# Optimization experiments

Hardware: AMD Instinct MI355X
Metric: run time of the kernel (lower is better)

## Reference

```python
import jax, jax.numpy as jnp
import numpy as np

BIG = 3.4028234e+38  # torch fill value used as additive mask
EPS = 1e-5           # nn.LayerNorm default eps


def _layernorm(x):
    mu = jnp.mean(x, axis=-1, keepdims=True)
    var = jnp.mean(jnp.square(x - mu), axis=-1, keepdims=True)
    return (x - mu) / jnp.sqrt(var + EPS)


def setup_inputs() -> dict:
    key = jax.random.key(0)
    ks = jax.random.split(key, 12)
    B, N, H, S = 32, 512, 256, 3  # batch, num_codes, embedding_size, num_stacks
    features = jax.random.normal(ks[0], (B, N, H), dtype=jnp.float32)
    masks = jnp.ones((B, N, 1), dtype=jnp.float32)
    guide = jax.random.randint(ks[1], (B, N, N), 0, 2).astype(jnp.float32)
    prior_guide = jax.random.uniform(ks[2], (B, N, N), dtype=jnp.float32)
    sc = 0.02
    WQ = jax.random.normal(ks[3], (S, H, H), dtype=jnp.float32) * sc
    WK = jax.random.normal(ks[4], (S, H, H), dtype=jnp.float32) * sc
    WV = jax.random.normal(ks[5], (S, H, H), dtype=jnp.float32) * sc
    W1 = jax.random.normal(ks[6], (S, H, H), dtype=jnp.float32) * sc
    b1 = jnp.zeros((S, H), dtype=jnp.float32)
    W2 = jax.random.normal(ks[7], (S, H, H), dtype=jnp.float32) * sc
    b2 = jnp.zeros((S, H), dtype=jnp.float32)
    return {"features": features, "masks": masks, "guide": guide,
            "prior_guide": prior_guide, "WQ": WQ, "WK": WK, "WV": WV,
            "W1": W1, "b1": b1, "W2": W2, "b2": b2}


def reference(features, masks, guide, prior_guide, WQ, WK, WV, W1, b1, W2, b2):
    H = features.shape[-1]
    scale = 1.0 / jnp.sqrt(jnp.float32(H))
    attention_mask = jnp.where(masks[:, :, 0] != 0, 0.0, BIG)  # [B,N]
    inf_mask = jnp.where(guide != 0, 0.0, BIG)                 # [B,N,N]
    attentions = []
    x = features
    for i in range(WQ.shape[0]):
        f = masks * x                                          # [B,N,H]
        if i == 0:
            att = prior_guide[:, None, :, :]                   # use_prior path
        else:
            q = jnp.einsum('bnh,hd->bnd', f, WQ[i].T)          # nn.Linear: x @ W^T
            k = jnp.einsum('bnh,hd->bnd', f, WK[i].T)
            pre = jnp.einsum('bqd,bkd->bqk', q, k) * scale     # [B,N,N] (heads=1)
            pre = pre - attention_mask[:, None, :] - inf_mask
            att = jax.nn.softmax(pre, axis=-1)[:, None, :, :]  # [B,1,N,N]
        attentions.append(att)
        v = jnp.einsum('bnh,hd->bnd', f, WV[i].T)              # [B,N,H]
        post = jnp.einsum('bqk,bkh->bqh', att[:, 0], v)        # squeeze head dim
        post = _layernorm(post + f)
        ffn = jnp.maximum(jnp.einsum('bnh,hd->bnd', post, W1[i].T) + b1[i], 0.0)
        ffn = jnp.einsum('bnh,hd->bnd', ffn, W2[i].T) + b2[i]
        x = _layernorm(ffn + post)
    return x * masks, jnp.stack(attentions)
```

## Files before the change

kernel.cpp:

```cpp
#include <hip/hip_runtime.h>
#include <cstdint>
#include <cstddef>

#define B_ 32
#define N_ 512
#define H_ 256
#define S_ 3
#define BN_ (B_*N_)
#define HH_ (H_*H_)
#define BIGF 3.4028234e+38f
#define EPSF 1e-5f

typedef __bf16 bf16x8 __attribute__((ext_vector_type(8)));
typedef float  f32x4  __attribute__((ext_vector_type(4)));

typedef const void __attribute__((address_space(1)))* gas_t;
typedef void __attribute__((address_space(3)))* las_t;

__device__ __forceinline__ void async16(const unsigned short* g, unsigned short* l) {
  __builtin_amdgcn_global_load_lds((gas_t)g, (las_t)l, 16, 0, 0);
}

__device__ __forceinline__ unsigned short f2bf(float f) {
  __bf16 h = (__bf16)f;
  unsigned short s;
  __builtin_memcpy(&s, &h, 2);
  return s;
}
__device__ __forceinline__ float bf2f(unsigned short u) {
  unsigned int v = ((unsigned int)u) << 16;
  float f;
  __builtin_memcpy(&f, &v, 4);
  return f;
}

#define KC_STAGE(lane) ((((lane) & 3) ^ (((lane) >> 3) & 3)) * 8)
#define KC_READ(quad, l15) ((((quad) ^ (((l15) >> 1) & 3))) * 8)

__global__ __launch_bounds__(256) void cvt_all_k(
    const float* __restrict__ WQ, const float* __restrict__ WK,
    const float* __restrict__ WV, const float* __restrict__ W1,
    const float* __restrict__ W2,
    unsigned short* __restrict__ wqk, unsigned short* __restrict__ wv,
    unsigned short* __restrict__ w1, unsigned short* __restrict__ w2) {
  const int per = S_ * HH_ / 4;
  int gi = blockIdx.x * 256 + threadIdx.x;
  int which = gi / per;
  int e4 = gi - which * per;
  float4 v;
  if      (which == 0) v = ((const float4*)WQ)[e4];
  else if (which == 1) v = ((const float4*)WK)[e4];
  else if (which == 2) v = ((const float4*)WV)[e4];
  else if (which == 3) v = ((const float4*)W1)[e4];
  else                 v = ((const float4*)W2)[e4];
  ushort4 o;
  o.x = f2bf(v.x); o.y = f2bf(v.y); o.z = f2bf(v.z); o.w = f2bf(v.w);
  int e = e4 * 4;
  if (which <= 1) {
    int L = e / HH_, off = e - L * HH_;
    *(ushort4*)&wqk[(size_t)L * 2 * HH_ + (which == 1 ? HH_ : 0) + off] = o;
  } else if (which == 2) ((ushort4*)wv)[e4] = o;
  else if   (which == 3) ((ushort4*)w1)[e4] = o;
  else                   ((ushort4*)w2)[e4] = o;
}

__global__ __launch_bounds__(256) void mask_mul_k(
    const float* __restrict__ x, const float* __restrict__ masks,
    unsigned short* __restrict__ fb) {
  int i = blockIdx.x * 256 + threadIdx.x;
  int row = i >> 6;
  float m = masks[row];
  float4 v = ((const float4*)x)[i];
  ushort4 o;
  o.x = f2bf(v.x * m); o.y = f2bf(v.y * m); o.z = f2bf(v.z * m); o.w = f2bf(v.w * m);
  ((ushort4*)fb)[i] = o;
}

__global__ __launch_bounds__(256) void mfma_gemm_k(
    const unsigned short* __restrict__ A, const unsigned short* __restrict__ Bm,
    unsigned short* __restrict__ Cb,
    int K, int Nn, int lda, int ldb, long sA, long sB, long sC) {
  __shared__ __align__(16) unsigned short As[2][128 * 32];
  __shared__ __align__(16) unsigned short Bs[2][128 * 32];
  const int b = blockIdx.z;
  const int t = threadIdx.x;
  const int wave = t >> 6, lane = t & 63;
  const int wm = wave >> 1, wn = wave & 1;
  const int quad = lane >> 4, l15 = lane & 15;
  const int m0 = blockIdx.y * 128, n0 = blockIdx.x * 128;
  const int srow = lane >> 2;
  const int kc = KC_STAGE(lane);
  const int pos8 = (lane & 3) * 8;

  const unsigned short* pa0 = A + (size_t)b * sA + (size_t)(m0 + wave * 32 + srow) * lda + kc;
  const unsigned short* pa1 = pa0 + 16 * (size_t)lda;
  const unsigned short* pb0 = Bm + (size_t)b * sB + (size_t)(n0 + wave * 32 + srow) * ldb + kc;
  const unsigned short* pb1 = pb0 + 16 * (size_t)ldb;
  const int lo = (wave * 32 + srow) * 32 + pos8;

  f32x4 acc[4][4];
#pragma unroll
  for (int i = 0; i < 4; ++i)
#pragma unroll
    for (int j = 0; j < 4; ++j) acc[i][j] = (f32x4){0.f, 0.f, 0.f, 0.f};

  const int soff = KC_READ(quad, l15);
  const int NT = K >> 5;
  async16(pa0, &As[0][lo]); async16(pa1, &As[0][lo + 16 * 32]);
  async16(pb0, &Bs[0][lo]); async16(pb1, &Bs[0][lo + 16 * 32]);
  __syncthreads();
  int cur = 0;
  for (int tt = 0; tt < NT; ++tt) {
    if (tt + 1 < NT) {
      const int kn = (tt + 1) << 5;
      async16(pa0 + kn, &As[cur ^ 1][lo]); async16(pa1 + kn, &As[cur ^ 1][lo + 16 * 32]);
      async16(pb0 + kn, &Bs[cur ^ 1][lo]); async16(pb1 + kn, &Bs[cur ^ 1][lo + 16 * 32]);
    }
    bf16x8 af[4], bfr[4];
#pragma unroll
    for (int i = 0; i < 4; ++i)
      af[i] = *(const bf16x8*)&As[cur][(wm * 64 + i * 16 + l15) * 32 + soff];
#pragma unroll
    for (int j = 0; j < 4; ++j)
      bfr[j] = *(const bf16x8*)&Bs[cur][(wn * 64 + j * 16 + l15) * 32 + soff];
#pragma unroll
    for (int i = 0; i < 4; ++i)
#pragma unroll
      for (int j = 0; j < 4; ++j)
        acc[i][j] = __builtin_amdgcn_mfma_f32_16x16x32_bf16(af[i], bfr[j], acc[i][j], 0, 0, 0);
    __syncthreads();
    cur ^= 1;
  }

#pragma unroll
  for (int i = 0; i < 4; ++i) {
    const int rbase = m0 + wm * 64 + i * 16 + quad * 4;
#pragma unroll
    for (int j = 0; j < 4; ++j) {
      const int c = n0 + wn * 64 + j * 16 + l15;
#pragma unroll
      for (int r = 0; r < 4; ++r)
        Cb[(size_t)b * sC + (size_t)(rbase + r) * Nn + c] = f2bf(acc[i][j][r]);
    }
  }
}

template<int PRIOR>
__global__ __launch_bounds__(512) void ls_pv_k(
    const unsigned short* __restrict__ qk, const float* __restrict__ prior,
    const float* __restrict__ masks, const float* __restrict__ guide,
    const unsigned short* __restrict__ vT, const unsigned short* __restrict__ resb,
    float* __restrict__ att, float* __restrict__ post, unsigned short* __restrict__ postb) {
  __shared__ __align__(16) unsigned short As[2][64 * 32];
  __shared__ __align__(16) unsigned short Bs[2][512 * 32];
  __shared__ __align__(16) unsigned short Ps[64 * 520];
  __shared__ float red[4][64][2];
  const int b = blockIdx.x;
  const int t = threadIdx.x;
  const int wave = t >> 6, lane = t & 63;
  const int quad = lane >> 4, l15 = lane & 15;
  const int m0 = blockIdx.y * 64;
  const int srow = lane >> 2;
  const int kc = KC_STAGE(lane);
  const int pos8 = (lane & 3) * 8;
  const int soff = KC_READ(quad, l15);

  const unsigned short* vb = vT + (size_t)b * H_ * N_;
  const unsigned short* pv0 = vb + (size_t)(wave * 16 + srow) * N_ + kc;
  const unsigned short* pv1 = pv0 + (size_t)128 * N_;
  const int lvo = (wave * 16 + srow) * 32 + pos8;

  if (PRIOR) {
    async16(pv0, &Bs[0][lvo]);
    async16(pv1, &Bs[0][lvo + 128 * 32]);
    const float* src = prior + ((size_t)b * N_ + m0) * N_;
    float*       dst = att   + ((size_t)b * N_ + m0) * N_;
#pragma unroll
    for (int s = 0; s < 16; ++s) {
      int idx4 = s * 512 + t;
      float4 v = ((const float4*)src)[idx4];
      ((float4*)dst)[idx4] = v;
      int row = idx4 >> 7, col4 = idx4 & 127;
      ushort4 o;
      o.x = f2bf(v.x); o.y = f2bf(v.y); o.z = f2bf(v.z); o.w = f2bf(v.w);
      *(ushort4*)&Ps[row * 520 + col4 * 4] = o;
    }
    __syncthreads();
  } else {
    const int wm = wave >> 2, wn = wave & 3;
    const int ld = 2 * H_;
    const unsigned short* base = qk + (size_t)b * N_ * ld;
    const unsigned short* pa = base + (size_t)(m0 + wave * 16 + srow) * ld + kc;
    const unsigned short* pb = base + H_ + (size_t)(wave * 64 + srow) * ld + kc;
    const int lao = (wave * 16 + srow) * 32 + pos8;
    const int lbo = (wave * 64 + srow) * 32 + pos8;

    f32x4 acc[2][8];
#pragma unroll
    for (int i = 0; i < 2; ++i)
#pragma unroll
      for (int j = 0; j < 8; ++j) acc[i][j] = (f32x4){0.f, 0.f, 0.f, 0.f};

    if (wave < 4) async16(pa, &As[0][lao]);
#pragma unroll
    for (int c = 0; c < 4; ++c)
      async16(pb + (size_t)c * 16 * ld, &Bs[0][lbo + c * 16 * 32]);
    __syncthreads();
    int cur = 0;
#pragma unroll
    for (int tt = 0; tt < 8; ++tt) {
      if (tt < 7) {
        const int kn = (tt + 1) * 32;
        if (wave < 4) async16(pa + kn, &As[cur ^ 1][lao]);
#pragma unroll
        for (int c = 0; c < 4; ++c)
          async16(pb + (size_t)c * 16 * ld + kn, &Bs[cur ^ 1][lbo + c * 16 * 32]);
      }
      bf16x8 af[2], bfr[8];
#pragma unroll
      for (int i = 0; i < 2; ++i)
        af[i] = *(const bf16x8*)&As[cur][(wm * 32 + i * 16 + l15) * 32 + soff];
#pragma unroll
      for (int j = 0; j < 8; ++j)
        bfr[j] = *(const bf16x8*)&Bs[cur][(wn * 128 + j * 16 + l15) * 32 + soff];
#pragma unroll
      for (int i = 0; i < 2; ++i)
#pragma unroll
        for (int j = 0; j < 8; ++j)
          acc[i][j] = __builtin_amdgcn_mfma_f32_16x16x32_bf16(af[i], bfr[j], acc[i][j], 0, 0, 0);
      __syncthreads();
      cur ^= 1;
    }

    async16(pv0, &Bs[0][lvo]);
    async16(pv1, &Bs[0][lvo + 128 * 32]);

    float am[8];
#pragma unroll
    for (int j = 0; j < 8; ++j) {
      float mv = masks[(size_t)b * N_ + wn * 128 + j * 16 + l15];
      am[j] = (mv != 0.f) ? 0.f : BIGF;
    }
#pragma unroll
    for (int i = 0; i < 2; ++i) {
#pragma unroll
      for (int r = 0; r < 4; ++r) {
        const int mloc = wm * 32 + i * 16 + quad * 4 + r;
        const float* gr = guide + ((size_t)b * N_ + m0 + mloc) * N_;
        float mx = -BIGF;
#pragma unroll
        for (int j = 0; j < 8; ++j) {
          const int c = wn * 128 + j * 16 + l15;
          float g = gr[c];
          float v = acc[i][j][r] * 0.0625f - am[j] - ((g != 0.f) ? 0.f : BIGF);
          acc[i][j][r] = v;
          mx = fmaxf(mx, v);
        }
#pragma unroll
        for (int off = 1; off < 16; off <<= 1) mx = fmaxf(mx, __shfl_xor(mx, off));
        if (l15 == 0) red[wn][mloc][0] = mx;
      }
    }
    __syncthreads();
#pragma unroll
    for (int i = 0; i < 2; ++i) {
#pragma unroll
      for (int r = 0; r < 4; ++r) {
        const int mloc = wm * 32 + i * 16 + quad * 4 + r;
        float M = fmaxf(fmaxf(red[0][mloc][0], red[1][mloc][0]),
                        fmaxf(red[2][mloc][0], red[3][mloc][0]));
        float s = 0.f;
#pragma unroll
        for (int j = 0; j < 8; ++j) {
          float e = __expf(acc[i][j][r] - M);
          acc[i][j][r] = e;
          s += e;
        }
#pragma unroll
        for (int off = 1; off < 16; off <<= 1) s += __shfl_xor(s, off);
        if (l15 == 0) red[wn][mloc][1] = s;
      }
    }
    __syncthreads();
#pragma unroll
    for (int i = 0; i < 2; ++i) {
#pragma unroll
      for (int r = 0; r < 4; ++r) {
        const int mloc = wm * 32 + i * 16 + quad * 4 + r;
        float S = red[0][mloc][1] + red[1][mloc][1] + red[2][mloc][1] + red[3][mloc][1];
        float inv = 1.f / S;
        const size_t rowoff = ((size_t)b * N_ + m0 + mloc) * N_;
#pragma unroll
        for (int j = 0; j < 8; ++j) {
          const int c = wn * 128 + j * 16 + l15;
          float o = acc[i][j][r] * inv;
          att[rowoff + c] = o;
          Ps[mloc * 520 + c] = f2bf(o);
        }
      }
    }
    __syncthreads();
  }

  const int wm2 = wave >> 2, wn2 = wave & 3;

  f32x4 acc2[2][4];
#pragma unroll
  for (int i = 0; i < 2; ++i)
#pragma unroll
    for (int j = 0; j < 4; ++j) acc2[i][j] = (f32x4){0.f, 0.f, 0.f, 0.f};

  int cur = 0;
#pragma unroll
  for (int tt = 0; tt < 16; ++tt) {
    if (tt < 15) {
      const int kn = (tt + 1) * 32;
      async16(pv0 + kn, &Bs[cur ^ 1][lvo]);
      async16(pv1 + kn, &Bs[cur ^ 1][lvo + 128 * 32]);
    }
    bf16x8 af[2], bfr[4];
#pragma unroll
    for (int i = 0; i < 2; ++i)
      af[i] = *(const bf16x8*)&Ps[(wm2 * 32 + i * 16 + l15) * 520 + tt * 32 + quad * 8];
#pragma unroll
    for (int j = 0; j < 4; ++j)
      bfr[j] = *(const bf16x8*)&Bs[cur][(wn2 * 64 + j * 16 + l15) * 32 + soff];
#pragma unroll
    for (int i = 0; i < 2; ++i)
#pragma unroll
      for (int j = 0; j < 4; ++j)
        acc2[i][j] = __builtin_amdgcn_mfma_f32_16x16x32_bf16(af[i], bfr[j], acc2[i][j], 0, 0, 0);
    __syncthreads();
    cur ^= 1;
  }

#pragma unroll
  for (int i = 0; i < 2; ++i) {
#pragma unroll
    for (int r = 0; r < 4; ++r) {
      const int mloc = wm2 * 32 + i * 16 + quad * 4 + r;
      const long grow = (long)b * N_ + m0 + mloc;
      float s = 0.f, q = 0.f;
#pragma unroll
      for (int j = 0; j < 4; ++j) {
        const int c = wn2 * 64 + j * 16 + l15;
        float v = acc2[i][j][r] + bf2f(resb[grow * H_ + c]);
        acc2[i][j][r] = v;
        s += v; q += v * v;
      }
#pragma unroll
      for (int off = 1; off < 16; off <<= 1) {
        s += __shfl_xor(s, off);
        q += __shfl_xor(q, off);
      }
      if (l15 == 0) { red[wn2][mloc][0] = s; red[wn2][mloc][1] = q; }
    }
  }
  __syncthreads();
#pragma unroll
  for (int i = 0; i < 2; ++i) {
#pragma unroll
    for (int r = 0; r < 4; ++r) {
      const int mloc = wm2 * 32 + i * 16 + quad * 4 + r;
      const long grow = (long)b * N_ + m0 + mloc;
      float S = red[0][mloc][0] + red[1][mloc][0] + red[2][mloc][0] + red[3][mloc][0];
      float Q = red[0][mloc][1] + red[1][mloc][1] + red[2][mloc][1] + red[3][mloc][1];
      float mu = S * (1.f / H_);
      float var = Q * (1.f / H_) - mu * mu;
      float inv = 1.f / sqrtf(var + EPSF);
#pragma unroll
      for (int j = 0; j < 4; ++j) {
        const int c = wn2 * 64 + j * 16 + l15;
        float o = (acc2[i][j][r] - mu) * inv;
        post[grow * H_ + c] = o;
        postb[grow * H_ + c] = f2bf(o);
      }
    }
  }
}

template<int LAST>
__global__ __launch_bounds__(512) void ffn_k(
    const unsigned short* __restrict__ postb, const float* __restrict__ postf,
    const unsigned short* __restrict__ w1, const float* __restrict__ b1,
    const unsigned short* __restrict__ w2, const float* __restrict__ b2,
    const float* __restrict__ masks,
    unsigned short* __restrict__ fb, float* __restrict__ outx) {
  __shared__ __align__(16) unsigned short As[2][64 * 32];
  __shared__ __align__(16) unsigned short Bs[2][256 * 32];
  __shared__ __align__(16) unsigned short T1[64 * 264];
  __shared__ float red[4][64][2];
  const int t = threadIdx.x;
  const int wave = t >> 6, lane = t & 63;
  const int wm = wave >> 2, wn = wave & 3;
  const int quad = lane >> 4, l15 = lane & 15;
  const int m0 = blockIdx.y * 64;
  const int srow = lane >> 2;
  const int kc = KC_STAGE(lane);
  const int pos8 = (lane & 3) * 8;
  const int soff = KC_READ(quad, l15);

  const unsigned short* pa = postb + (size_t)(m0 + wave * 16 + srow) * H_ + kc;
  const int lao = (wave * 16 + srow) * 32 + pos8;
  const int lbo = (wave * 16 + srow) * 32 + pos8;

  const unsigned short* qb0 = w2 + (size_t)(wave * 16 + srow) * H_ + kc;
  const unsigned short* qb1 = qb0 + (size_t)128 * H_;

  {
    const unsigned short* pb0 = w1 + (size_t)(wave * 16 + srow) * H_ + kc;
    const unsigned short* pb1 = pb0 + (size_t)128 * H_;
    f32x4 acc[2][4];
#pragma unroll
    for (int i = 0; i < 2; ++i)
#pragma unroll
      for (int j = 0; j < 4; ++j) acc[i][j] = (f32x4){0.f, 0.f, 0.f, 0.f};
    if (wave < 4) async16(pa, &As[0][lao]);
    async16(pb0, &Bs[0][lbo]);
    async16(pb1, &Bs[0][lbo + 128 * 32]);
    __syncthreads();
    int cur = 0;
#pragma unroll
    for (int tt = 0; tt < 8; ++tt) {
      if (tt < 7) {
        const int kn = (tt + 1) * 32;
        if (wave < 4) async16(pa + kn, &As[cur ^ 1][lao]);
        async16(pb0 + kn, &Bs[cur ^ 1][lbo]);
        async16(pb1 + kn, &Bs[cur ^ 1][lbo + 128 * 32]);
      }
      bf16x8 af[2], bfr[4];
#pragma unroll
      for (int i = 0; i < 2; ++i)
        af[i] = *(const bf16x8*)&As[cur][(wm * 32 + i * 16 + l15) * 32 + soff];
#pragma unroll
      for (int j = 0; j < 4; ++j)
        bfr[j] = *(const bf16x8*)&Bs[cur][(wn * 64 + j * 16 + l15) * 32 + soff];
#pragma unroll
      for (int i = 0; i < 2; ++i)
#pragma unroll
        for (int j = 0; j < 4; ++j)
          acc[i][j] = __builtin_amdgcn_mfma_f32_16x16x32_bf16(af[i], bfr[j], acc[i][j], 0, 0, 0);
      __syncthreads();
      cur ^= 1;
    }

    async16(qb0, &Bs[0][lbo]);
    async16(qb1, &Bs[0][lbo + 128 * 32]);

    float bv[4];
#pragma unroll
    for (int j = 0; j < 4; ++j) bv[j] = b1[wn * 64 + j * 16 + l15];
#pragma unroll
    for (int i = 0; i < 2; ++i) {
#pragma unroll
      for (int r = 0; r < 4; ++r) {
        const int mloc = wm * 32 + i * 16 + quad * 4 + r;
#pragma unroll
        for (int j = 0; j < 4; ++j) {
          const int c = wn * 64 + j * 16 + l15;
          T1[mloc * 264 + c] = f2bf(fmaxf(acc[i][j][r] + bv[j], 0.f));
        }
      }
    }
  }
  __syncthreads();

  {
    f32x4 acc[2][4];
#pragma unroll
    for (int i = 0; i < 2; ++i)
#pragma unroll
      for (int j = 0; j < 4; ++j) acc[i][j] = (f32x4){0.f, 0.f, 0.f, 0.f};
    int cur = 0;
#pragma unroll
    for (int tt = 0; tt < 8; ++tt) {
      if (tt < 7) {
        const int kn = (tt + 1) * 32;
        async16(qb0 + kn, &Bs[cur ^ 1][lbo]);
        async16(qb1 + kn, &Bs[cur ^ 1][lbo + 128 * 32]);
      }
      bf16x8 af[2], bfr[4];
#pragma unroll
      for (int i = 0; i < 2; ++i)
        af[i] = *(const bf16x8*)&T1[(wm * 32 + i * 16 + l15) * 264 + tt * 32 + quad * 8];
#pragma unroll
      for (int j = 0; j < 4; ++j)
        bfr[j] = *(const bf16x8*)&Bs[cur][(wn * 64 + j * 16 + l15) * 32 + soff];
#pragma unroll
      for (int i = 0; i < 2; ++i)
#pragma unroll
        for (int j = 0; j < 4; ++j)
          acc[i][j] = __builtin_amdgcn_mfma_f32_16x16x32_bf16(af[i], bfr[j], acc[i][j], 0, 0, 0);
      __syncthreads();
      cur ^= 1;
    }
    float bv[4];
#pragma unroll
    for (int j = 0; j < 4; ++j) bv[j] = b2[wn * 64 + j * 16 + l15];
#pragma unroll
    for (int i = 0; i < 2; ++i) {
#pragma unroll
      for (int r = 0; r < 4; ++r) {
        const int mloc = wm * 32 + i * 16 + quad * 4 + r;
        const long grow = (long)m0 + mloc;
        float s = 0.f, q = 0.f;
#pragma unroll
        for (int j = 0; j < 4; ++j) {
          const int c = wn * 64 + j * 16 + l15;
          float v = acc[i][j][r] + bv[j] + postf[grow * H_ + c];
          acc[i][j][r] = v;
          s += v; q += v * v;
        }
#pragma unroll
        for (int off = 1; off < 16; off <<= 1) {
          s += __shfl_xor(s, off);
          q += __shfl_xor(q, off);
        }
        if (l15 == 0) { red[wn][mloc][0] = s; red[wn][mloc][1] = q; }
      }
    }
    __syncthreads();
#pragma unroll
    for (int i = 0; i < 2; ++i) {
#pragma unroll
      for (int r = 0; r < 4; ++r) {
        const int mloc = wm * 32 + i * 16 + quad * 4 + r;
        const long grow = (long)m0 + mloc;
        float S = red[0][mloc][0] + red[1][mloc][0] + red[2][mloc][0] + red[3][mloc][0];
        float Q = red[0][mloc][1] + red[1][mloc][1] + red[2][mloc][1] + red[3][mloc][1];
        float mu = S * (1.f / H_);
        float var = Q * (1.f / H_) - mu * mu;
        float inv = 1.f / sqrtf(var + EPSF);
        float mval = masks[grow];
#pragma unroll
        for (int j = 0; j < 4; ++j) {
          const int c = wn * 64 + j * 16 + l15;
          float o = (acc[i][j][r] - mu) * inv * mval;
          if (LAST) outx[grow * H_ + c] = o;
          else      fb[grow * H_ + c] = f2bf(o);
        }
      }
    }
  }
}

extern "C" void kernel_launch(void* const* d_in, const int* in_sizes, int n_in,
                              void* d_out, int out_size, void* d_ws, size_t ws_size,
                              hipStream_t stream) {
  const float* features = (const float*)d_in[0];
  const float* masks    = (const float*)d_in[1];
  const float* guide    = (const float*)d_in[2];
  const float* prior    = (const float*)d_in[3];
  const float* WQ       = (const float*)d_in[4];
  const float* WK       = (const float*)d_in[5];
  const float* WV       = (const float*)d_in[6];
  const float* W1       = (const float*)d_in[7];
  const float* b1       = (const float*)d_in[8];
  const float* W2       = (const float*)d_in[9];
  const float* b2       = (const float*)d_in[10];

  float* out     = (float*)d_out;
  float* out_x   = out;
  float* out_att = out + (size_t)BN_ * H_;

  char* w = (char*)d_ws;
  float* post = (float*)w;                     w += (size_t)BN_ * H_ * 4;
  unsigned short* f_bf   = (unsigned short*)w; w += (size_t)BN_ * H_ * 2;
  unsigned short* qk_bf  = (unsigned short*)w; w += (size_t)BN_ * 2 * H_ * 2;
  unsigned short* post_bf= (unsigned short*)w; w += (size_t)BN_ * H_ * 2;
  unsigned short* vT     = (unsigned short*)w; w += (size_t)BN_ * H_ * 2;
  unsigned short* wqk_bf = (unsigned short*)w; w += (size_t)S_ * 2 * HH_ * 2;
  unsigned short* wv_bf  = (unsigned short*)w; w += (size_t)S_ * HH_ * 2;
  unsigned short* w1_bf  = (unsigned short*)w; w += (size_t)S_ * HH_ * 2;
  unsigned short* w2_bf  = (unsigned short*)w; w += (size_t)S_ * HH_ * 2;

  dim3 g_cvt(5 * S_ * HH_ / 1024);
  dim3 g_ew(BN_ * H_ / 1024);
  dim3 g_qkp(4, BN_ / 128, 1);
  dim3 g_vt(4, 2, B_);
  dim3 g_ls(B_, N_ / 64, 1);
  dim3 g_ffn(1, BN_ / 64, 1);

  cvt_all_k<<<g_cvt, 256, 0, stream>>>(WQ, WK, WV, W1, W2, wqk_bf, wv_bf, w1_bf, w2_bf);
  mask_mul_k<<<g_ew, 256, 0, stream>>>(features, masks, f_bf);

  const long sF  = (long)N_ * H_;
  const long sVT = (long)H_ * N_;

  for (int i = 0; i < S_; ++i) {
    float* att = out_att + (size_t)i * B_ * N_ * N_;
    mfma_gemm_k<<<g_vt, 256, 0, stream>>>(wv_bf + (size_t)i * HH_, f_bf, vT,
                                          H_, N_, H_, H_, 0, sF, sVT);
    if (i == 0) {
      ls_pv_k<1><<<g_ls, 512, 0, stream>>>(nullptr, prior, nullptr, nullptr,
                                           vT, f_bf, att, post, post_bf);
    } else {
      mfma_gemm_k<<<g_qkp, 256, 0, stream>>>(f_bf, wqk_bf + (size_t)i * 2 * HH_, qk_bf,
                                             H_, 2 * H_, H_, H_, 0, 0, 0);
      ls_pv_k<0><<<g_ls, 512, 0, stream>>>(qk_bf, nullptr, masks, guide,
                                           vT, f_bf, att, post, post_bf);
    }
    if (i < S_ - 1) {
      ffn_k<0><<<g_ffn, 512, 0, stream>>>(post_bf, post,
          w1_bf + (size_t)i * HH_, b1 + (size_t)i * H_,
          w2_bf + (size_t)i * HH_, b2 + (size_t)i * H_, masks, f_bf, nullptr);
    } else {
      ffn_k<1><<<g_ffn, 512, 0, stream>>>(post_bf, post,
          w1_bf + (size_t)i * HH_, b1 + (size_t)i * H_,
          w2_bf + (size_t)i * HH_, b2 + (size_t)i * H_, masks, nullptr, out_x);
    }
  }
}
```

Before: 377.8 us.

## Split softmax and PV into separate kernels, merge QK and V GEMMs, shrink tiles

The fused softmax+PV kernel is split in two. ls_k writes the softmax probabilities to a bf16 workspace buffer, and pv_k reads them back. The prior path becomes a standalone convert kernel. The QK projection and V projection GEMMs are merged into a single launch (gemm2_k). Row tiles for ls, pv and ffn shrink from 64 to 32 rows, with launch bounds raised to 4 blocks per CU. The aim is more blocks and higher occupancy in place of the large shared-memory P tile. The cost is an extra round trip of the B×N×N bf16 probability matrix through global memory.

```diff
diff --git a/kernel.cpp b/kernel.cpp
--- a/kernel.cpp
+++ b/kernel.cpp
@@ -10,6 +10,8 @@
 #define HH_ (H_*H_)
 #define BIGF 3.4028234e+38f
 #define EPSF 1e-5f
+#define SF_ ((long)N_ * H_)
+#define SVT_ ((long)H_ * N_)
 
 typedef __bf16 bf16x8 __attribute__((ext_vector_type(8)));
 typedef float  f32x4  __attribute__((ext_vector_type(4)));
@@ -76,18 +78,26 @@
   ((ushort4*)fb)[i] = o;
 }
 
-__global__ __launch_bounds__(256) void mfma_gemm_k(
+__global__ __launch_bounds__(512) void prior_cvt_k(
+    const float* __restrict__ prior, float* __restrict__ att,
+    unsigned short* __restrict__ pbf) {
+  size_t i = (size_t)blockIdx.x * 512 + threadIdx.x;
+  float4 v = ((const float4*)prior)[i];
+  ((float4*)att)[i] = v;
+  ushort4 o;
+  o.x = f2bf(v.x); o.y = f2bf(v.y); o.z = f2bf(v.z); o.w = f2bf(v.w);
+  ((ushort4*)pbf)[i] = o;
+}
+
+__device__ __forceinline__ void gemm_body(
     const unsigned short* __restrict__ A, const unsigned short* __restrict__ Bm,
     unsigned short* __restrict__ Cb,
-    int K, int Nn, int lda, int ldb, long sA, long sB, long sC) {
-  __shared__ __align__(16) unsigned short As[2][128 * 32];
-  __shared__ __align__(16) unsigned short Bs[2][128 * 32];
-  const int b = blockIdx.z;
-  const int t = threadIdx.x;
+    int K, int Nn, int lda, int ldb, long sA, long sB, long sC,
+    int b, int m0, int n0, int t,
+    unsigned short (&As)[2][128 * 32], unsigned short (&Bs)[2][128 * 32]) {
   const int wave = t >> 6, lane = t & 63;
   const int wm = wave >> 1, wn = wave & 1;
   const int quad = lane >> 4, l15 = lane & 15;
-  const int m0 = blockIdx.y * 128, n0 = blockIdx.x * 128;
   const int srow = lane >> 2;
   const int kc = KC_STAGE(lane);
   const int pos8 = (lane & 3) * 8;
@@ -145,191 +155,220 @@
   }
 }
 
-template<int PRIOR>
-__global__ __launch_bounds__(512) void ls_pv_k(
-    const unsigned short* __restrict__ qk, const float* __restrict__ prior,
-    const float* __restrict__ masks, const float* __restrict__ guide,
-    const unsigned short* __restrict__ vT, const unsigned short* __restrict__ resb,
-    float* __restrict__ att, float* __restrict__ post, unsigned short* __restrict__ postb) {
-  __shared__ __align__(16) unsigned short As[2][64 * 32];
+__global__ __launch_bounds__(256) void mfma_gemm_k(
+    const unsigned short* __restrict__ A, const unsigned short* __restrict__ Bm,
+    unsigned short* __restrict__ Cb,
+    int K, int Nn, int lda, int ldb, long sA, long sB, long sC) {
+  __shared__ __align__(16) unsigned short As[2][128 * 32];
+  __shared__ __align__(16) unsigned short Bs[2][128 * 32];
+  gemm_body(A, Bm, Cb, K, Nn, lda, ldb, sA, sB, sC,
+            blockIdx.z, blockIdx.y * 128, blockIdx.x * 128, threadIdx.x, As, Bs);
+}
+
+__global__ __launch_bounds__(256) void gemm2_k(
+    const unsigned short* __restrict__ A1, const unsigned short* __restrict__ B1,
+    unsigned short* __restrict__ C1,
+    const unsigned short* __restrict__ A2, const unsigned short* __restrict__ B2,
+    unsigned short* __restrict__ C2) {
+  __shared__ __align__(16) unsigned short As[2][128 * 32];
+  __shared__ __align__(16) unsigned short Bs[2][128 * 32];
+  const int bx = blockIdx.x;
+  if (bx < 512) {
+    gemm_body(A1, B1, C1, H_, 2 * H_, H_, H_, 0, 0, 0,
+              0, (bx >> 2) * 128, (bx & 3) * 128, threadIdx.x, As, Bs);
+  } else {
+    const int v = bx - 512;
+    gemm_body(A2, B2, C2, H_, N_, H_, H_, 0, SF_, SVT_,
+              v >> 3, ((v >> 2) & 1) * 128, (v & 3) * 128, threadIdx.x, As, Bs);
+  }
+}
+
+__global__ __launch_bounds__(512, 4) void ls_k(
+    const unsigned short* __restrict__ qk, const float* __restrict__ masks,
+    const float* __restrict__ guide,
+    float* __restrict__ att, unsigned short* __restrict__ pbf) {
+  __shared__ __align__(16) unsigned short As[2][32 * 32];
   __shared__ __align__(16) unsigned short Bs[2][512 * 32];
-  __shared__ __align__(16) unsigned short Ps[64 * 520];
-  __shared__ float red[4][64][2];
+  __shared__ float red[8][32][2];
   const int b = blockIdx.x;
+  const int m0 = blockIdx.y * 32;
   const int t = threadIdx.x;
   const int wave = t >> 6, lane = t & 63;
   const int quad = lane >> 4, l15 = lane & 15;
-  const int m0 = blockIdx.y * 64;
   const int srow = lane >> 2;
   const int kc = KC_STAGE(lane);
   const int pos8 = (lane & 3) * 8;
   const int soff = KC_READ(quad, l15);
-
-  const unsigned short* vb = vT + (size_t)b * H_ * N_;
-  const unsigned short* pv0 = vb + (size_t)(wave * 16 + srow) * N_ + kc;
-  const unsigned short* pv1 = pv0 + (size_t)128 * N_;
-  const int lvo = (wave * 16 + srow) * 32 + pos8;
-
-  if (PRIOR) {
-    async16(pv0, &Bs[0][lvo]);
-    async16(pv1, &Bs[0][lvo + 128 * 32]);
-    const float* src = prior + ((size_t)b * N_ + m0) * N_;
-    float*       dst = att   + ((size_t)b * N_ + m0) * N_;
-#pragma unroll
-    for (int s = 0; s < 16; ++s) {
-      int idx4 = s * 512 + t;
-      float4 v = ((const float4*)src)[idx4];
-      ((float4*)dst)[idx4] = v;
-      int row = idx4 >> 7, col4 = idx4 & 127;
-      ushort4 o;
-      o.x = f2bf(v.x); o.y = f2bf(v.y); o.z = f2bf(v.z); o.w = f2bf(v.w);
-      *(ushort4*)&Ps[row * 520 + col4 * 4] = o;
-    }
+  const int ld = 2 * H_;
+
+  const unsigned short* base = qk + (size_t)b * N_ * ld;
+  const unsigned short* pa = base + (size_t)(m0 + wave * 16 + srow) * ld + kc;
+  const unsigned short* pb = base + H_ + (size_t)(wave * 64 + srow) * ld + kc;
+  const int lao = (wave * 16 + srow) * 32 + pos8;
+  const int lbo = (wave * 64 + srow) * 32 + pos8;
+
+  f32x4 acc[2][4];
+#pragma unroll
+  for (int i = 0; i < 2; ++i)
+#pragma unroll
+    for (int j = 0; j < 4; ++j) acc[i][j] = (f32x4){0.f, 0.f, 0.f, 0.f};
+
+  if (wave < 2) async16(pa, &As[0][lao]);
+#pragma unroll
+  for (int c = 0; c < 4; ++c)
+    async16(pb + (size_t)c * 16 * ld, &Bs[0][lbo + c * 16 * 32]);
+  __syncthreads();
+  int cur = 0;
+#pragma unroll
+  for (int tt = 0; tt < 8; ++tt) {
+    if (tt < 7) {
+      const int kn = (tt + 1) * 32;
+      if (wave < 2) async16(pa + kn, &As[cur ^ 1][lao]);
+#pragma unroll
+      for (int c = 0; c < 4; ++c)
+        async16(pb + (size_t)c * 16 * ld + kn, &Bs[cur ^ 1][lbo + c * 16 * 32]);
+    }
+    bf16x8 af[2], bfr[4];
+#pragma unroll
+    for (int i = 0; i < 2; ++i)
+      af[i] = *(const bf16x8*)&As[cur][(i * 16 + l15) * 32 + soff];
+#pragma unroll
+    for (int j = 0; j < 4; ++j)
+      bfr[j] = *(const bf16x8*)&Bs[cur][(wave * 64 + j * 16 + l15) * 32 + soff];
+#pragma unroll
+    for (int i = 0; i < 2; ++i)
+#pragma unroll
+      for (int j = 0; j < 4; ++j)
+        acc[i][j] = __builtin_amdgcn_mfma_f32_16x16x32_bf16(af[i], bfr[j], acc[i][j], 0, 0, 0);
     __syncthreads();
-  } else {
-    const int wm = wave >> 2, wn = wave & 3;
-    const int ld = 2 * H_;
-    const unsigned short* base = qk + (size_t)b * N_ * ld;
-    const unsigned short* pa = base + (size_t)(m0 + wave * 16 + srow) * ld + kc;
-    const unsigned short* pb = base + H_ + (size_t)(wave * 64 + srow) * ld + kc;
-    const int lao = (wave * 16 + srow) * 32 + pos8;
-    const int lbo = (wave * 64 + srow) * 32 + pos8;
-
-    f32x4 acc[2][8];
-#pragma unroll
-    for (int i = 0; i < 2; ++i)
-#pragma unroll
-      for (int j = 0; j < 8; ++j) acc[i][j] = (f32x4){0.f, 0.f, 0.f, 0.f};
-
-    if (wave < 4) async16(pa, &As[0][lao]);
-#pragma unroll
-    for (int c = 0; c < 4; ++c)
-      async16(pb + (size_t)c * 16 * ld, &Bs[0][lbo + c * 16 * 32]);
-    __syncthreads();
-    int cur = 0;
-#pragma unroll
-    for (int tt = 0; tt < 8; ++tt) {
-      if (tt < 7) {
-        const int kn = (tt + 1) * 32;
-        if (wave < 4) async16(pa + kn, &As[cur ^ 1][lao]);
-#pragma unroll
-        for (int c = 0; c < 4; ++c)
-          async16(pb + (size_t)c * 16 * ld + kn, &Bs[cur ^ 1][lbo + c * 16 * 32]);
-      }
-      bf16x8 af[2], bfr[8];
-#pragma unroll
-      for (int i = 0; i < 2; ++i)
-        af[i] = *(const bf16x8*)&As[cur][(wm * 32 + i * 16 + l15) * 32 + soff];
-#pragma unroll
-      for (int j = 0; j < 8; ++j)
-        bfr[j] = *(const bf16x8*)&Bs[cur][(wn * 128 + j * 16 + l15) * 32 + soff];
-#pragma unroll
-      for (int i = 0; i < 2; ++i)
-#pragma unroll
-        for (int j = 0; j < 8; ++j)
-          acc[i][j] = __builtin_amdgcn_mfma_f32_16x16x32_bf16(af[i], bfr[j], acc[i][j], 0, 0, 0);
-      __syncthreads();
-      cur ^= 1;
-    }
-
-    async16(pv0, &Bs[0][lvo]);
-    async16(pv1, &Bs[0][lvo + 128 * 32]);
-
-    float am[8];
-#pragma unroll
-    for (int j = 0; j < 8; ++j) {
-      float mv = masks[(size_t)b * N_ + wn * 128 + j * 16 + l15];
-      am[j] = (mv != 0.f) ? 0.f : BIGF;
-    }
-#pragma unroll
-    for (int i = 0; i < 2; ++i) {
-#pragma unroll
-      for (int r = 0; r < 4; ++r) {
-        const int mloc = wm * 32 + i * 16 + quad * 4 + r;
-        const float* gr = guide + ((size_t)b * N_ + m0 + mloc) * N_;
-        float mx = -BIGF;
-#pragma unroll
-        for (int j = 0; j < 8; ++j) {
-          const int c = wn * 128 + j * 16 + l15;
-          float g = gr[c];
-          float v = acc[i][j][r] * 0.0625f - am[j] - ((g != 0.f) ? 0.f : BIGF);
-          acc[i][j][r] = v;
-          mx = fmaxf(mx, v);
-        }
-#pragma unroll
-        for (int off = 1; off < 16; off <<= 1) mx = fmaxf(mx, __shfl_xor(mx, off));
-        if (l15 == 0) red[wn][mloc][0] = mx;
-      }
-    }
-    __syncthreads();
-#pragma unroll
-    for (int i = 0; i < 2; ++i) {
-#pragma unroll
-      for (int r = 0; r < 4; ++r) {
-        const int mloc = wm * 32 + i * 16 + quad * 4 + r;
-        float M = fmaxf(fmaxf(red[0][mloc][0], red[1][mloc][0]),
-                        fmaxf(red[2][mloc][0], red[3][mloc][0]));
-        float s = 0.f;
-#pragma unroll
-        for (int j = 0; j < 8; ++j) {
-          float e = __expf(acc[i][j][r] - M);
-          acc[i][j][r] = e;
-          s += e;
-        }
-#pragma unroll
-        for (int off = 1; off < 16; off <<= 1) s += __shfl_xor(s, off);
-        if (l15 == 0) red[wn][mloc][1] = s;
-      }
-    }
-    __syncthreads();
-#pragma unroll
-    for (int i = 0; i < 2; ++i) {
-#pragma unroll
-      for (int r = 0; r < 4; ++r) {
-        const int mloc = wm * 32 + i * 16 + quad * 4 + r;
-        float S = red[0][mloc][1] + red[1][mloc][1] + red[2][mloc][1] + red[3][mloc][1];
-        float inv = 1.f / S;
-        const size_t rowoff = ((size_t)b * N_ + m0 + mloc) * N_;
-#pragma unroll
-        for (int j = 0; j < 8; ++j) {
-          const int c = wn * 128 + j * 16 + l15;
-          float o = acc[i][j][r] * inv;
-          att[rowoff + c] = o;
-          Ps[mloc * 520 + c] = f2bf(o);
-        }
-      }
-    }
-    __syncthreads();
-  }
-
-  const int wm2 = wave >> 2, wn2 = wave & 3;
-
-  f32x4 acc2[2][4];
+    cur ^= 1;
+  }
+
+  float am[4];
+#pragma unroll
+  for (int j = 0; j < 4; ++j) {
+    float mv = masks[(size_t)b * N_ + wave * 64 + j * 16 + l15];
+    am[j] = (mv != 0.f) ? 0.f : BIGF;
+  }
+#pragma unroll
+  for (int i = 0; i < 2; ++i) {
+#pragma unroll
+    for (int r = 0; r < 4; ++r) {
+      const int rloc = i * 16 + quad * 4 + r;
+      const float* gr = guide + ((size_t)b * N_ + m0 + rloc) * N_;
+      float mx = -BIGF;
+#pragma unroll
+      for (int j = 0; j < 4; ++j) {
+        const int c = wave * 64 + j * 16 + l15;
+        float g = gr[c];
+        float v = acc[i][j][r] * 0.0625f - am[j] - ((g != 0.f) ? 0.f : BIGF);
+        acc[i][j][r] = v;
+        mx = fmaxf(mx, v);
+      }
+#pragma unroll
+      for (int off = 1; off < 16; off <<= 1) mx = fmaxf(mx, __shfl_xor(mx, off));
+      if (l15 == 0) red[wave][rloc][0] = mx;
+    }
+  }
+  __syncthreads();
+#pragma unroll
+  for (int i = 0; i < 2; ++i) {
+#pragma unroll
+    for (int r = 0; r < 4; ++r) {
+      const int rloc = i * 16 + quad * 4 + r;
+      float M = red[0][rloc][0];
+#pragma unroll
+      for (int w = 1; w < 8; ++w) M = fmaxf(M, red[w][rloc][0]);
+      float s = 0.f;
+#pragma unroll
+      for (int j = 0; j < 4; ++j) {
+        float e = __expf(acc[i][j][r] - M);
+        acc[i][j][r] = e;
+        s += e;
+      }
+#pragma unroll
+      for (int off = 1; off < 16; off <<= 1) s += __shfl_xor(s, off);
+      if (l15 == 0) red[wave][rloc][1] = s;
+    }
+  }
+  __syncthreads();
+#pragma unroll
+  for (int i = 0; i < 2; ++i) {
+#pragma unroll
+    for (int r = 0; r < 4; ++r) {
+      const int rloc = i * 16 + quad * 4 + r;
+      float S = red[0][rloc][1];
+#pragma unroll
+      for (int w = 1; w < 8; ++w) S += red[w][rloc][1];
+      float inv = 1.f / S;
+      const size_t rowg = (size_t)b * N_ + m0 + rloc;
+#pragma unroll
+      for (int j = 0; j < 4; ++j) {
+        const int c = wave * 64 + j * 16 + l15;
+        float o = acc[i][j][r] * inv;
+        att[rowg * N_ + c] = o;
+        pbf[rowg * N_ + c] = f2bf(o);
+      }
+    }
+  }
+}
+
+__global__ __launch_bounds__(256, 4) void pv_k(
+    const unsigned short* __restrict__ pbf, const unsigned short* __restrict__ vT,
+    const unsigned short* __restrict__ resb,
+    float* __restrict__ post, unsigned short* __restrict__ postb) {
+  __shared__ __align__(16) unsigned short As[2][32 * 32];
+  __shared__ __align__(16) unsigned short Bs[2][256 * 32];
+  __shared__ float red[4][32][2];
+  const int b = blockIdx.x;
+  const int m0b = blockIdx.y * 32;
+  const long grow0 = (long)b * N_ + m0b;
+  const int t = threadIdx.x;
+  const int wave = t >> 6, lane = t & 63;
+  const int quad = lane >> 4, l15 = lane & 15;
+  const int srow = lane >> 2;
+  const int kc = KC_STAGE(lane);
+  const int pos8 = (lane & 3) * 8;
+  const int soff = KC_READ(quad, l15);
+
+  const unsigned short* pa = pbf + (size_t)(grow0 + wave * 16 + srow) * N_ + kc;
+  const unsigned short* pb = vT + (size_t)b * SVT_ + (size_t)(wave * 16 + srow) * N_ + kc;
+  const int lao = (wave * 16 + srow) * 32 + pos8;
+  const int lbo = (wave * 16 + srow) * 32 + pos8;
+
+  f32x4 acc[2][4];
 #pragma unroll
   for (int i = 0; i < 2; ++i)
 #pragma unroll
-    for (int j = 0; j < 4; ++j) acc2[i][j] = (f32x4){0.f, 0.f, 0.f, 0.f};
-
+    for (int j = 0; j < 4; ++j) acc[i][j] = (f32x4){0.f, 0.f, 0.f, 0.f};
+
+  if (wave < 2) async16(pa, &As[0][lao]);
+#pragma unroll
+  for (int c = 0; c < 4; ++c)
+    async16(pb + (size_t)c * 64 * N_, &Bs[0][lbo + c * 64 * 32]);
+  __syncthreads();
   int cur = 0;
 #pragma unroll
   for (int tt = 0; tt < 16; ++tt) {
     if (tt < 15) {
       const int kn = (tt + 1) * 32;
-      async16(pv0 + kn, &Bs[cur ^ 1][lvo]);
-      async16(pv1 + kn, &Bs[cur ^ 1][lvo + 128 * 32]);
+      if (wave < 2) async16(pa + kn, &As[cur ^ 1][lao]);
+#pragma unroll
+      for (int c = 0; c < 4; ++c)
+        async16(pb + (size_t)c * 64 * N_ + kn, &Bs[cur ^ 1][lbo + c * 64 * 32]);
     }
     bf16x8 af[2], bfr[4];
 #pragma unroll
     for (int i = 0; i < 2; ++i)
-      af[i] = *(const bf16x8*)&Ps[(wm2 * 32 + i * 16 + l15) * 520 + tt * 32 + quad * 8];
+      af[i] = *(const bf16x8*)&As[cur][(i * 16 + l15) * 32 + soff];
 #pragma unroll
     for (int j = 0; j < 4; ++j)
-      bfr[j] = *(const bf16x8*)&Bs[cur][(wn2 * 64 + j * 16 + l15) * 32 + soff];
+      bfr[j] = *(const bf16x8*)&Bs[cur][(wave * 64 + j * 16 + l15) * 32 + soff];
 #pragma unroll
     for (int i = 0; i < 2; ++i)
 #pragma unroll
       for (int j = 0; j < 4; ++j)
-        acc2[i][j] = __builtin_amdgcn_mfma_f32_16x16x32_bf16(af[i], bfr[j], acc2[i][j], 0, 0, 0);
+        acc[i][j] = __builtin_amdgcn_mfma_f32_16x16x32_bf16(af[i], bfr[j], acc[i][j], 0, 0, 0);
     __syncthreads();
     cur ^= 1;
   }
@@ -338,14 +377,14 @@
   for (int i = 0; i < 2; ++i) {
 #pragma unroll
     for (int r = 0; r < 4; ++r) {
-      const int mloc = wm2 * 32 + i * 16 + quad * 4 + r;
-      const long grow = (long)b * N_ + m0 + mloc;
+      const int rloc = i * 16 + quad * 4 + r;
+      const long grow = grow0 + rloc;
       float s = 0.f, q = 0.f;
 #pragma unroll
       for (int j = 0; j < 4; ++j) {
-        const int c = wn2 * 64 + j * 16 + l15;
-        float v = acc2[i][j][r] + bf2f(resb[grow * H_ + c]);
-        acc2[i][j][r] = v;
+        const int c = wave * 64 + j * 16 + l15;
+        float v = acc[i][j][r] + bf2f(resb[grow * H_ + c]);
+        acc[i][j][r] = v;
         s += v; q += v * v;
       }
 #pragma unroll
@@ -353,7 +392,7 @@
         s += __shfl_xor(s, off);
         q += __shfl_xor(q, off);
       }
-      if (l15 == 0) { red[wn2][mloc][0] = s; red[wn2][mloc][1] = q; }
+      if (l15 == 0) { red[wave][rloc][0] = s; red[wave][rloc][1] = q; }
     }
   }
   __syncthreads();
@@ -361,17 +400,17 @@
   for (int i = 0; i < 2; ++i) {
 #pragma unroll
     for (int r = 0; r < 4; ++r) {
-      const int mloc = wm2 * 32 + i * 16 + quad * 4 + r;
-      const long grow = (long)b * N_ + m0 + mloc;
-      float S = red[0][mloc][0] + red[1][mloc][0] + red[2][mloc][0] + red[3][mloc][0];
-      float Q = red[0][mloc][1] + red[1][mloc][1] + red[2][mloc][1] + red[3][mloc][1];
+      const int rloc = i * 16 + quad * 4 + r;
+      const long grow = grow0 + rloc;
+      float S = red[0][rloc][0] + red[1][rloc][0] + red[2][rloc][0] + red[3][rloc][0];
+      float Q = red[0][rloc][1] + red[1][rloc][1] + red[2][rloc][1] + red[3][rloc][1];
       float mu = S * (1.f / H_);
       float var = Q * (1.f / H_) - mu * mu;
       float inv = 1.f / sqrtf(var + EPSF);
 #pragma unroll
       for (int j = 0; j < 4; ++j) {
-        const int c = wn2 * 64 + j * 16 + l15;
-        float o = (acc2[i][j][r] - mu) * inv;
+        const int c = wave * 64 + j * 16 + l15;
+        float o = (acc[i][j][r] - mu) * inv;
         post[grow * H_ + c] = o;
         postb[grow * H_ + c] = f2bf(o);
       }
@@ -380,21 +419,20 @@
 }
 
 template<int LAST>
-__global__ __launch_bounds__(512) void ffn_k(
+__global__ __launch_bounds__(256, 2) void ffn_k(
     const unsigned short* __restrict__ postb, const float* __restrict__ postf,
     const unsigned short* __restrict__ w1, const float* __restrict__ b1,
     const unsigned short* __restrict__ w2, const float* __restrict__ b2,
     const float* __restrict__ masks,
     unsigned short* __restrict__ fb, float* __restrict__ outx) {
-  __shared__ __align__(16) unsigned short As[2][64 * 32];
+  __shared__ __align__(16) unsigned short As[2][32 * 32];
   __shared__ __align__(16) unsigned short Bs[2][256 * 32];
-  __shared__ __align__(16) unsigned short T1[64 * 264];
-  __shared__ float red[4][64][2];
+  __shared__ __align__(16) unsigned short T1[32 * 264];
+  __shared__ float red[4][32][2];
   const int t = threadIdx.x;
   const int wave = t >> 6, lane = t & 63;
-  const int wm = wave >> 2, wn = wave & 3;
   const int quad = lane >> 4, l15 = lane & 15;
-  const int m0 = blockIdx.y * 64;
+  const int m0 = blockIdx.y * 32;
   const int srow = lane >> 2;
   const int kc = KC_STAGE(lane);
   const int pos8 = (lane & 3) * 8;
@@ -404,37 +442,37 @@
   const int lao = (wave * 16 + srow) * 32 + pos8;
   const int lbo = (wave * 16 + srow) * 32 + pos8;
 
-  const unsigned short* qb0 = w2 + (size_t)(wave * 16 + srow) * H_ + kc;
-  const unsigned short* qb1 = qb0 + (size_t)128 * H_;
+  const unsigned short* qb = w2 + (size_t)(wave * 16 + srow) * H_ + kc;
 
   {
-    const unsigned short* pb0 = w1 + (size_t)(wave * 16 + srow) * H_ + kc;
-    const unsigned short* pb1 = pb0 + (size_t)128 * H_;
+    const unsigned short* pb = w1 + (size_t)(wave * 16 + srow) * H_ + kc;
     f32x4 acc[2][4];
 #pragma unroll
     for (int i = 0; i < 2; ++i)
 #pragma unroll
       for (int j = 0; j < 4; ++j) acc[i][j] = (f32x4){0.f, 0.f, 0.f, 0.f};
-    if (wave < 4) async16(pa, &As[0][lao]);
-    async16(pb0, &Bs[0][lbo]);
-    async16(pb1, &Bs[0][lbo + 128 * 32]);
+    if (wave < 2) async16(pa, &As[0][lao]);
+#pragma unroll
+    for (int c = 0; c < 4; ++c)
+      async16(pb + (size_t)c * 64 * H_, &Bs[0][lbo + c * 64 * 32]);
     __syncthreads();
     int cur = 0;
 #pragma unroll
     for (int tt = 0; tt < 8; ++tt) {
       if (tt < 7) {
         const int kn = (tt + 1) * 32;
-        if (wave < 4) async16(pa + kn, &As[cur ^ 1][lao]);
-        async16(pb0 + kn, &Bs[cur ^ 1][lbo]);
-        async16(pb1 + kn, &Bs[cur ^ 1][lbo + 128 * 32]);
+        if (wave < 2) async16(pa + kn, &As[cur ^ 1][lao]);
+#pragma unroll
+        for (int c = 0; c < 4; ++c)
+          async16(pb + (size_t)c * 64 * H_ + kn, &Bs[cur ^ 1][lbo + c * 64 * 32]);
       }
       bf16x8 af[2], bfr[4];
 #pragma unroll
       for (int i = 0; i < 2; ++i)
-        af[i] = *(const bf16x8*)&As[cur][(wm * 32 + i * 16 + l15) * 32 + soff];
+        af[i] = *(const bf16x8*)&As[cur][(i * 16 + l15) * 32 + soff];
 #pragma unroll
       for (int j = 0; j < 4; ++j)
-        bfr[j] = *(const bf16x8*)&Bs[cur][(wn * 64 + j * 16 + l15) * 32 + soff];
+        bfr[j] = *(const bf16x8*)&Bs[cur][(wave * 64 + j * 16 + l15) * 32 + soff];
 #pragma unroll
       for (int i = 0; i < 2; ++i)
 #pragma unroll
@@ -444,21 +482,22 @@
       cur ^= 1;
     }
 
-    async16(qb0, &Bs[0][lbo]);
-    async16(qb1, &Bs[0][lbo + 128 * 32]);
+#pragma unroll
+    for (int c = 0; c < 4; ++c)
+      async16(qb + (size_t)c * 64 * H_, &Bs[0][lbo + c * 64 * 32]);
 
     float bv[4];
 #pragma unroll
-    for (int j = 0; j < 4; ++j) bv[j] = b1[wn * 64 + j * 16 + l15];
+    for (int j = 0; j < 4; ++j) bv[j] = b1[wave * 64 + j * 16 + l15];
 #pragma unroll
     for (int i = 0; i < 2; ++i) {
 #pragma unroll
       for (int r = 0; r < 4; ++r) {
-        const int mloc = wm * 32 + i * 16 + quad * 4 + r;
+        const int rloc = i * 16 + quad * 4 + r;
 #pragma unroll
         for (int j = 0; j < 4; ++j) {
-          const int c = wn * 64 + j * 16 + l15;
-          T1[mloc * 264 + c] = f2bf(fmaxf(acc[i][j][r] + bv[j], 0.f));
+          const int c = wave * 64 + j * 16 + l15;
+          T1[rloc * 264 + c] = f2bf(fmaxf(acc[i][j][r] + bv[j], 0.f));
         }
       }
     }
@@ -476,16 +515,17 @@
     for (int tt = 0; tt < 8; ++tt) {
       if (tt < 7) {
         const int kn = (tt + 1) * 32;
-        async16(qb0 + kn, &Bs[cur ^ 1][lbo]);
-        async16(qb1 + kn, &Bs[cur ^ 1][lbo + 128 * 32]);
+#pragma unroll
+        for (int c = 0; c < 4; ++c)
+          async16(qb + (size_t)c * 64 * H_ + kn, &Bs[cur ^ 1][lbo + c * 64 * 32]);
       }
       bf16x8 af[2], bfr[4];
 #pragma unroll
       for (int i = 0; i < 2; ++i)
-        af[i] = *(const bf16x8*)&T1[(wm * 32 + i * 16 + l15) * 264 + tt * 32 + quad * 8];
+        af[i] = *(const bf16x8*)&T1[(i * 16 + l15) * 264 + tt * 32 + quad * 8];
 #pragma unroll
       for (int j = 0; j < 4; ++j)
-        bfr[j] = *(const bf16x8*)&Bs[cur][(wn * 64 + j * 16 + l15) * 32 + soff];
+        bfr[j] = *(const bf16x8*)&Bs[cur][(wave * 64 + j * 16 + l15) * 32 + soff];
 #pragma unroll
       for (int i = 0; i < 2; ++i)
 #pragma unroll
@@ -496,17 +536,17 @@
     }
     float bv[4];
 #pragma unroll
-    for (int j = 0; j < 4; ++j) bv[j] = b2[wn * 64 + j * 16 + l15];
+    for (int j = 0; j < 4; ++j) bv[j] = b2[wave * 64 + j * 16 + l15];
 #pragma unroll
     for (int i = 0; i < 2; ++i) {
 #pragma unroll
       for (int r = 0; r < 4; ++r) {
-        const int mloc = wm * 32 + i * 16 + quad * 4 + r;
-        const long grow = (long)m0 + mloc;
+        const int rloc = i * 16 + quad * 4 + r;
+        const long grow = (long)m0 + rloc;
         float s = 0.f, q = 0.f;
 #pragma unroll
         for (int j = 0; j < 4; ++j) {
-          const int c = wn * 64 + j * 16 + l15;
+          const int c = wave * 64 + j * 16 + l15;
           float v = acc[i][j][r] + bv[j] + postf[grow * H_ + c];
           acc[i][j][r] = v;
           s += v; q += v * v;
@@ -516,7 +556,7 @@
           s += __shfl_xor(s, off);
           q += __shfl_xor(q, off);
         }
-        if (l15 == 0) { red[wn][mloc][0] = s; red[wn][mloc][1] = q; }
+        if (l15 == 0) { red[wave][rloc][0] = s; red[wave][rloc][1] = q; }
       }
     }
     __syncthreads();
@@ -524,17 +564,17 @@
     for (int i = 0; i < 2; ++i) {
 #pragma unroll
       for (int r = 0; r < 4; ++r) {
-        const int mloc = wm * 32 + i * 16 + quad * 4 + r;
-        const long grow = (long)m0 + mloc;
-        float S = red[0][mloc][0] + red[1][mloc][0] + red[2][mloc][0] + red[3][mloc][0];
-        float Q = red[0][mloc][1] + red[1][mloc][1] + red[2][mloc][1] + red[3][mloc][1];
+        const int rloc = i * 16 + quad * 4 + r;
+        const long grow = (long)m0 + rloc;
+        float S = red[0][rloc][0] + red[1][rloc][0] + red[2][rloc][0] + red[3][rloc][0];
+        float Q = red[0][rloc][1] + red[1][rloc][1] + red[2][rloc][1] + red[3][rloc][1];
         float mu = S * (1.f / H_);
         float var = Q * (1.f / H_) - mu * mu;
         float inv = 1.f / sqrtf(var + EPSF);
         float mval = masks[grow];
 #pragma unroll
         for (int j = 0; j < 4; ++j) {
-          const int c = wn * 64 + j * 16 + l15;
+          const int c = wave * 64 + j * 16 + l15;
           float o = (acc[i][j][r] - mu) * inv * mval;
           if (LAST) outx[grow * H_ + c] = o;
           else      fb[grow * H_ + c] = f2bf(o);
@@ -569,6 +609,7 @@
   unsigned short* qk_bf  = (unsigned short*)w; w += (size_t)BN_ * 2 * H_ * 2;
   unsigned short* post_bf= (unsigned short*)w; w += (size_t)BN_ * H_ * 2;
   unsigned short* vT     = (unsigned short*)w; w += (size_t)BN_ * H_ * 2;
+  unsigned short* p_bf   = (unsigned short*)w; w += (size_t)BN_ * N_ * 2;
   unsigned short* wqk_bf = (unsigned short*)w; w += (size_t)S_ * 2 * HH_ * 2;
   unsigned short* wv_bf  = (unsigned short*)w; w += (size_t)S_ * HH_ * 2;
   unsigned short* w1_bf  = (unsigned short*)w; w += (size_t)S_ * HH_ * 2;
@@ -576,36 +617,33 @@
 
   dim3 g_cvt(5 * S_ * HH_ / 1024);
   dim3 g_ew(BN_ * H_ / 1024);
-  dim3 g_qkp(4, BN_ / 128, 1);
   dim3 g_vt(4, 2, B_);
-  dim3 g_ls(B_, N_ / 64, 1);
-  dim3 g_ffn(1, BN_ / 64, 1);
+  dim3 g_g2(768);
+  dim3 g_pc(B_ * N_ * N_ / 4 / 512);
+  dim3 g_ls(B_, N_ / 32);
+  dim3 g_pv(B_, N_ / 32);
+  dim3 g_ffn(1, BN_ / 32);
 
   cvt_all_k<<<g_cvt, 256, 0, stream>>>(WQ, WK, WV, W1, W2, wqk_bf, wv_bf, w1_bf, w2_bf);
   mask_mul_k<<<g_ew, 256, 0, stream>>>(features, masks, f_bf);
 
-  const long sF  = (long)N_ * H_;
-  const long sVT = (long)H_ * N_;
-
   for (int i = 0; i < S_; ++i) {
     float* att = out_att + (size_t)i * B_ * N_ * N_;
-    mfma_gemm_k<<<g_vt, 256, 0, stream>>>(wv_bf + (size_t)i * HH_, f_bf, vT,
-                                          H_, N_, H_, H_, 0, sF, sVT);
     if (i == 0) {
-      ls_pv_k<1><<<g_ls, 512, 0, stream>>>(nullptr, prior, nullptr, nullptr,
-                                           vT, f_bf, att, post, post_bf);
+      mfma_gemm_k<<<g_vt, 256, 0, stream>>>(wv_bf, f_bf, vT, H_, N_, H_, H_, 0, SF_, SVT_);
+      prior_cvt_k<<<g_pc, 512, 0, stream>>>(prior, att, p_bf);
     } else {
-      mfma_gemm_k<<<g_qkp, 256, 0, stream>>>(f_bf, wqk_bf + (size_t)i * 2 * HH_, qk_bf,
-                                             H_, 2 * H_, H_, H_, 0, 0, 0);
-      ls_pv_k<0><<<g_ls, 512, 0, stream>>>(qk_bf, nullptr, masks, guide,
-                                           vT, f_bf, att, post, post_bf);
-    }
+      gemm2_k<<<g_g2, 256, 0, stream>>>(f_bf, wqk_bf + (size_t)i * 2 * HH_, qk_bf,
+                                        wv_bf + (size_t)i * HH_, f_bf, vT);
+      ls_k<<<g_ls, 512, 0, stream>>>(qk_bf, masks, guide, att, p_bf);
+    }
+    pv_k<<<g_pv, 256, 0, stream>>>(p_bf, vT, f_bf, post, post_bf);
     if (i < S_ - 1) {
-      ffn_k<0><<<g_ffn, 512, 0, stream>>>(post_bf, post,
+      ffn_k<0><<<g_ffn, 256, 0, stream>>>(post_bf, post,
           w1_bf + (size_t)i * HH_, b1 + (size_t)i * H_,
           w2_bf + (size_t)i * HH_, b2 + (size_t)i * H_, masks, f_bf, nullptr);
     } else {
-      ffn_k<1><<<g_ffn, 512, 0, stream>>>(post_bf, post,
+      ffn_k<1><<<g_ffn, 256, 0, stream>>>(post_bf, post,
           w1_bf + (size_t)i * HH_, b1 + (size_t)i * H_,
           w2_bf + (size_t)i * HH_, b2 + (size_t)i * H_, masks, nullptr, out_x);
     }
```

Measured after the change: 399.7 us. +5.8%, slower.
